# Performance work log

Measured on AMD Instinct MI355X. Metric: run time of the kernel, lower is better.

The kernel has to match this reference:

```python
import jax, jax.numpy as jnp
import numpy as np

NEG_INF = -1e9


def setup_inputs() -> dict:
    key = jax.random.key(0)
    k1, k2, k3, k4 = jax.random.split(key, 4)
    N, F_in, F_out = 8192, 512, 256
    features = jax.random.normal(k1, (N, F_in), dtype=jnp.float32)
    adj = jax.random.randint(k2, (N, N), 0, 2).astype(jnp.float32)
    W = jax.random.normal(k3, (F_in, F_out), dtype=jnp.float32) * 0.05
    a = jax.random.normal(k4, (2 * F_out,), dtype=jnp.float32) * 0.05
    return {"features": features, "adj": adj, "W": W, "a": a}


def reference(features, adj, W, a):
    # h = W @ features  -> [N, F_out]
    h = features @ W
    F_out = h.shape[1]
    a_src, a_dst = a[:F_out], a[F_out:]
    # a^T [h_i ; h_j] decomposes into per-node dot products (same math as
    # the concat+linear in the original, without the [N,N,2F] intermediate).
    e = jax.nn.leaky_relu((h @ a_src)[:, None] + (h @ a_dst)[None, :],
                          negative_slope=0.01)  # [N, N]
    masked_e = e + NEG_INF * (1.0 - adj)
    attention = jax.nn.softmax(masked_e, axis=1)  # row-wise over neighbors j
    output = attention @ h  # [N, F_out]
    return output, attention
```

## Files before the change

### kernel.cpp

```cpp
#include <hip/hip_runtime.h>
#include <hip/hip_bf16.h>

#define N 8192
#define FIN 512
#define FOUT 256

typedef __attribute__((ext_vector_type(8))) short bf16x8;
typedef __attribute__((ext_vector_type(4))) float f32x4;

__device__ __forceinline__ unsigned short f2bf(float x) {
  unsigned int u = __float_as_uint(x);
  return (unsigned short)((u + 0x7FFFu + ((u >> 16) & 1u)) >> 16);
}

__device__ __forceinline__ unsigned int pkbf2(float a, float b) {
  __hip_bfloat162 h = __float22bfloat162_rn(make_float2(a, b));
  unsigned int u;
  __builtin_memcpy(&u, &h, 4);
  return u;
}

__device__ __forceinline__ void load_lds16(const void* g, void* l) {
  __builtin_amdgcn_global_load_lds(
      (const __attribute__((address_space(1))) void*)g,
      (__attribute__((address_space(3))) void*)l, 16, 0, 0);
}

__global__ __launch_bounds__(256) void gat_k1_gemm_h(
    const float* __restrict__ A, const float* __restrict__ W,
    float* __restrict__ h, unsigned short* __restrict__ hT) {
  __shared__ __align__(16) float As[16][68];
  __shared__ __align__(16) float Bs[16][64];
  const int tid = threadIdx.x;
  const int tx = tid & 15, ty = tid >> 4;
  const int nb = blockIdx.x * 64, mb = blockIdx.y * 64;
  float acc[4][4] = {};
  for (int k0 = 0; k0 < FIN; k0 += 16) {
#pragma unroll
    for (int i = 0; i < 4; ++i) {
      int e = tid + 256 * i;
      int m = e >> 4, k = e & 15;
      As[k][m] = A[(size_t)(mb + m) * FIN + k0 + k];
      int n2 = e & 63, k2 = e >> 6;
      Bs[k2][n2] = W[(size_t)(k0 + k2) * FOUT + nb + n2];
    }
    __syncthreads();
#pragma unroll
    for (int k = 0; k < 16; ++k) {
      float4 av = *reinterpret_cast<const float4*>(&As[k][ty * 4]);
      float4 bv = *reinterpret_cast<const float4*>(&Bs[k][tx * 4]);
      float aa[4] = {av.x, av.y, av.z, av.w};
      float bb[4] = {bv.x, bv.y, bv.z, bv.w};
#pragma unroll
      for (int i = 0; i < 4; ++i)
#pragma unroll
        for (int j = 0; j < 4; ++j) acc[i][j] = fmaf(aa[i], bb[j], acc[i][j]);
    }
    __syncthreads();
  }
#pragma unroll
  for (int i = 0; i < 4; ++i) {
    int m = mb + ty * 4 + i;
#pragma unroll
    for (int j = 0; j < 4; ++j) {
      int n = nb + tx * 4 + j;
      h[(size_t)m * FOUT + n] = acc[i][j];
      hT[(size_t)n * N + m] = f2bf(acc[i][j]);
    }
  }
}

__global__ __launch_bounds__(256) void gat_k2_hshd(
    const float* __restrict__ h, const float* __restrict__ a,
    float* __restrict__ hs, float* __restrict__ hd, float* __restrict__ out) {
  const int gid = blockIdx.x * 256 + threadIdx.x;
  *reinterpret_cast<float4*>(out + (size_t)gid * 4) =
      make_float4(0.f, 0.f, 0.f, 0.f);

  const int wid = threadIdx.x >> 6;
  const int lane = threadIdx.x & 63;
  const int row = blockIdx.x * 4 + wid;
  float ps = 0.f, pd = 0.f;
#pragma unroll
  for (int i = 0; i < 4; ++i) {
    int c = lane + 64 * i;
    float v = h[(size_t)row * FOUT + c];
    ps += v * a[c];
    pd += v * a[FOUT + c];
  }
#pragma unroll
  for (int off = 32; off >= 1; off >>= 1) {
    ps += __shfl_down(ps, off);
    pd += __shfl_down(pd, off);
  }
  if (lane == 0) {
    hs[row] = ps;
    hd[row] = pd;
  }
}

__global__ __launch_bounds__(256) void gat_k3_attn(
    const float* __restrict__ adj, const float* __restrict__ hs,
    const float* __restrict__ hd, float* __restrict__ att,
    unsigned short* __restrict__ attB) {
  __shared__ __align__(16) float hd_s[N];
  __shared__ float red[4];
  const int tid = threadIdx.x;
  const int lane = tid & 63, wid = tid >> 6;
#pragma unroll
  for (int i = 0; i < 8; ++i) {
    int j = tid * 4 + 1024 * i;
    *reinterpret_cast<float4*>(&hd_s[j]) =
        *reinterpret_cast<const float4*>(&hd[j]);
  }
  __syncthreads();
  const int row0 = blockIdx.x * 8;
  for (int r = 0; r < 8; ++r) {
    const int row = row0 + r;
    const float hsv = hs[row];
    const float* arow = adj + (size_t)row * N;
    float4 l[8];
    float s = 0.f;
#pragma unroll
    for (int i = 0; i < 8; ++i) {
      int j = tid * 4 + 1024 * i;
      float4 a4 = *reinterpret_cast<const float4*>(&arow[j]);
      float4 h4 = *reinterpret_cast<const float4*>(&hd_s[j]);
      float x0 = hsv + h4.x, x1 = hsv + h4.y;
      float x2 = hsv + h4.z, x3 = hsv + h4.w;
      float4 e;
      e.x = (a4.x != 0.f) ? __expf(fmaxf(x0, 0.01f * x0)) : 0.f;
      e.y = (a4.y != 0.f) ? __expf(fmaxf(x1, 0.01f * x1)) : 0.f;
      e.z = (a4.z != 0.f) ? __expf(fmaxf(x2, 0.01f * x2)) : 0.f;
      e.w = (a4.w != 0.f) ? __expf(fmaxf(x3, 0.01f * x3)) : 0.f;
      l[i] = e;
      s += e.x + e.y + e.z + e.w;
    }
#pragma unroll
    for (int off = 32; off >= 1; off >>= 1) s += __shfl_down(s, off);
    if (lane == 0) red[wid] = s;
    __syncthreads();
    s = red[0] + red[1] + red[2] + red[3];
    __syncthreads();
    const float inv = 1.f / s;
    float* orow = att + (size_t)row * N;
    unsigned short* brow = attB ? attB + (size_t)row * N : nullptr;
#pragma unroll
    for (int i = 0; i < 8; ++i) {
      int j = tid * 4 + 1024 * i;
      float4 e = l[i];
      e.x *= inv; e.y *= inv; e.z *= inv; e.w *= inv;
      *reinterpret_cast<float4*>(&orow[j]) = e;
      if (brow) {
        uint2 pk;
        pk.x = pkbf2(e.x, e.y);
        pk.y = pkbf2(e.z, e.w);
        *reinterpret_cast<uint2*>(&brow[j]) = pk;
      }
    }
  }
}

__global__ __launch_bounds__(512, 4) void gat_k4_out(
    const unsigned short* __restrict__ attB,
    const unsigned short* __restrict__ hT, float* __restrict__ C) {
  __shared__ __align__(16) unsigned short Asb[3 * 64 * 64];
  __shared__ __align__(16) unsigned short Bsb[3 * 128 * 64];
  const int tid = threadIdx.x;
  const int lane = tid & 63;
  const int wid = tid >> 6;
  const int wm = wid & 1, wn = wid >> 1;
  const int g = lane >> 4, rsel = lane & 15;
  const int id = blockIdx.x;
  const int xcd = id & 7, pos = id >> 3;
  const int nh = xcd & 1, kq = (xcd >> 1) & 1, rh = xcd >> 2;
  const int row0 = (rh * 64 + pos) * 64;
  const int nb0 = nh * 128;
  const size_t kbase = (size_t)kq * 4096;

  const int ara = tid >> 3, asl = tid & 7;
  const unsigned short* asrc =
      attB + (size_t)(row0 + ara) * N + kbase + (asl ^ (ara & 7)) * 8;
  const int aofs = tid * 16;
  const unsigned short* bsrc[2];
  int bofs[2];
#pragma unroll
  for (int i = 0; i < 2; ++i) {
    int s = tid + 512 * i;
    int n = s >> 3, sl = s & 7;
    bsrc[i] = hT + (size_t)(nb0 + n) * N + kbase + (sl ^ (n & 7)) * 8;
    bofs[i] = s * 16;
  }

#define STAGE(T, BUF)                                                        \
  do {                                                                       \
    const int kel = (T) * 64;                                                \
    char* Ad = reinterpret_cast<char*>(Asb) + (BUF) * 8192;                  \
    char* Bd = reinterpret_cast<char*>(Bsb) + (BUF) * 16384;                 \
    load_lds16(asrc + kel, Ad + aofs);                                       \
    load_lds16(bsrc[0] + kel, Bd + bofs[0]);                                 \
    load_lds16(bsrc[1] + kel, Bd + bofs[1]);                                 \
  } while (0)

  f32x4 acc[2][2] = {};

  STAGE(0, 0);
  STAGE(1, 1);

  int cur = 0, stg = 2;
  for (int t = 0; t < 64; ++t) {
    if (t < 63)
      asm volatile("s_waitcnt vmcnt(3)" ::: "memory");
    else
      asm volatile("s_waitcnt vmcnt(0)" ::: "memory");
    __builtin_amdgcn_s_barrier();
    __builtin_amdgcn_sched_barrier(0);
    if (t < 62) STAGE(t + 2, stg);
    const char* Ac = reinterpret_cast<const char*>(Asb) + cur * 8192;
    const char* Bc = reinterpret_cast<const char*>(Bsb) + cur * 16384;
#pragma unroll
    for (int ks = 0; ks < 2; ++ks) {
      const int kg = ks * 4 + g;
      bf16x8 af[2], bg[2];
#pragma unroll
      for (int i = 0; i < 2; ++i) {
        int rr = wm * 32 + i * 16 + rsel;
        af[i] = *reinterpret_cast<const bf16x8*>(
            Ac + rr * 128 + ((kg ^ (rr & 7)) << 4));
        int n = wn * 32 + i * 16 + rsel;
        bg[i] = *reinterpret_cast<const bf16x8*>(
            Bc + n * 128 + ((kg ^ (n & 7)) << 4));
      }
#pragma unroll
      for (int i = 0; i < 2; ++i)
#pragma unroll
        for (int f = 0; f < 2; ++f)
          acc[i][f] = __builtin_amdgcn_mfma_f32_16x16x32_bf16(af[i], bg[f],
                                                              acc[i][f], 0, 0, 0);
    }
    cur = (cur == 2) ? 0 : cur + 1;
    stg = (stg == 2) ? 0 : stg + 1;
  }
#undef STAGE
#pragma unroll
  for (int i = 0; i < 2; ++i)
#pragma unroll
    for (int f = 0; f < 2; ++f)
#pragma unroll
      for (int r = 0; r < 4; ++r) {
        int row = row0 + wm * 32 + i * 16 + g * 4 + r;
        int col = nb0 + wn * 32 + f * 16 + rsel;
        atomicAdd(&C[(size_t)row * FOUT + col], acc[i][f][r]);
      }
}

__global__ __launch_bounds__(256, 4) void gat_k4_fb(
    const float* __restrict__ attF, const unsigned short* __restrict__ hT,
    float* __restrict__ C) {
  __shared__ __align__(16) unsigned short As[2][32 * 64];
  __shared__ __align__(16) unsigned short Bs[2][128 * 64];
  const int tid = threadIdx.x;
  const int lane = tid & 63;
  const int wn = tid >> 6;
  const int g = lane >> 4, rsel = lane & 15;
  const int id = blockIdx.x;
  const int xcd = id & 7, j = id >> 3;
  const int nh = xcd >> 2;
  const int row0 = ((xcd & 3) + 4 * j) * 32;
  const int nb0 = nh * 128;

  const float* asrcF[2];
  int awF[2];
#pragma unroll
  for (int i = 0; i < 2; ++i) {
    int e = tid + 256 * i;
    int r = e >> 4, p = e & 15;
    asrcF[i] = attF + (size_t)(row0 + r) * N + p * 4;
    awF[i] = r * 128 + ((((p >> 1) ^ (r & 7)) << 4)) + (p & 1) * 8;
  }
  const unsigned short* bsrc[4];
  int bofs[4];
#pragma unroll
  for (int i = 0; i < 4; ++i) {
    int s = tid + 256 * i;
    int n = s >> 3, sl = s & 7;
    bsrc[i] = hT + (size_t)(nb0 + n) * N + (sl ^ (n & 7)) * 8;
    bofs[i] = s * 16;
  }

  f32x4 acc[2][2] = {};
  float4 aF0, aF1;
  aF0 = *reinterpret_cast<const float4*>(asrcF[0]);
  aF1 = *reinterpret_cast<const float4*>(asrcF[1]);
  {
    uint2 pk;
    pk.x = pkbf2(aF0.x, aF0.y); pk.y = pkbf2(aF0.z, aF0.w);
    *reinterpret_cast<uint2*>(reinterpret_cast<char*>(As[0]) + awF[0]) = pk;
    pk.x = pkbf2(aF1.x, aF1.y); pk.y = pkbf2(aF1.z, aF1.w);
    *reinterpret_cast<uint2*>(reinterpret_cast<char*>(As[0]) + awF[1]) = pk;
  }
#pragma unroll
  for (int i = 0; i < 4; ++i)
    load_lds16(bsrc[i], reinterpret_cast<char*>(Bs[0]) + bofs[i]);
  __syncthreads();

  int cur = 0;
  for (int t = 0; t < 128; ++t) {
    if (t < 127) {
      const int kel = (t + 1) * 64;
      aF0 = *reinterpret_cast<const float4*>(asrcF[0] + kel);
      aF1 = *reinterpret_cast<const float4*>(asrcF[1] + kel);
#pragma unroll
      for (int i = 0; i < 4; ++i)
        load_lds16(bsrc[i] + kel, reinterpret_cast<char*>(Bs[cur ^ 1]) + bofs[i]);
    }
    const char* Ac = reinterpret_cast<const char*>(As[cur]);
    const char* Bc = reinterpret_cast<const char*>(Bs[cur]);
#pragma unroll
    for (int ks = 0; ks < 2; ++ks) {
      bf16x8 af[2], bg[2];
#pragma unroll
      for (int i = 0; i < 2; ++i) {
        int rr = i * 16 + rsel;
        af[i] = *reinterpret_cast<const bf16x8*>(
            Ac + rr * 128 + (((ks * 4 + g) ^ (rr & 7)) << 4));
        int n = wn * 32 + i * 16 + rsel;
        bg[i] = *reinterpret_cast<const bf16x8*>(
            Bc + n * 128 + (((ks * 4 + g) ^ (n & 7)) << 4));
      }
#pragma unroll
      for (int i = 0; i < 2; ++i)
#pragma unroll
        for (int f = 0; f < 2; ++f)
          acc[i][f] = __builtin_amdgcn_mfma_f32_16x16x32_bf16(af[i], bg[f],
                                                              acc[i][f], 0, 0, 0);
    }
    if (t < 127) {
      char* An = reinterpret_cast<char*>(As[cur ^ 1]);
      uint2 pk;
      pk.x = pkbf2(aF0.x, aF0.y); pk.y = pkbf2(aF0.z, aF0.w);
      *reinterpret_cast<uint2*>(An + awF[0]) = pk;
      pk.x = pkbf2(aF1.x, aF1.y); pk.y = pkbf2(aF1.z, aF1.w);
      *reinterpret_cast<uint2*>(An + awF[1]) = pk;
    }
    __syncthreads();
    if (t < 127) cur ^= 1;
  }
#pragma unroll
  for (int i = 0; i < 2; ++i)
#pragma unroll
    for (int f = 0; f < 2; ++f)
#pragma unroll
      for (int r = 0; r < 4; ++r) {
        int row = row0 + i * 16 + g * 4 + r;
        int col = nb0 + wn * 32 + f * 16 + rsel;
        C[(size_t)row * FOUT + col] = acc[i][f][r];
      }
}

extern "C" void kernel_launch(void* const* d_in, const int* in_sizes, int n_in,
                              void* d_out, int out_size, void* d_ws, size_t ws_size,
                              hipStream_t stream) {
  const float* features = (const float*)d_in[0];
  const float* adj = (const float*)d_in[1];
  const float* W = (const float*)d_in[2];
  const float* a = (const float*)d_in[3];

  float* out = (float*)d_out;
  float* att = out + (size_t)N * FOUT;

  char* ws = (char*)d_ws;
  float* h = (float*)ws;
  unsigned short* hT = (unsigned short*)(ws + (size_t)8388608);
  float* hs = (float*)(ws + (size_t)12582912);
  float* hd = hs + N;
  unsigned short* attB = (unsigned short*)(ws + (size_t)16777216);
  const size_t need = 16777216 + (size_t)N * N * 2;
  const bool useB = ws_size >= need;

  hipLaunchKernelGGL(gat_k1_gemm_h, dim3(FOUT / 64, N / 64), dim3(256), 0,
                     stream, features, W, h, hT);
  hipLaunchKernelGGL(gat_k2_hshd, dim3(N / 4), dim3(256), 0, stream, h, a, hs,
                     hd, out);
  hipLaunchKernelGGL(gat_k3_attn, dim3(N / 8), dim3(256), 0, stream, adj, hs,
                     hd, att, useB ? attB : nullptr);
  if (useB)
    hipLaunchKernelGGL(gat_k4_out, dim3(512), dim3(512), 0, stream, attB, hT,
                       out);
  else
    hipLaunchKernelGGL(gat_k4_fb, dim3(512), dim3(256), 0, stream, att, hT,
                       out);
}
```

Before: 264.3 us.

## Replace atomic split-K accumulation with per-split partial buffers and a reduction kernel

The attention·h GEMM now uses 128x128 output tiles with a 4-way K split. Each split writes plain stores into its own partial buffer instead of atomically adding into the zero-initialized output. A new reduction kernel sums the four partials, so the output no longer needs zeroing in the hs/hd kernel. The pipeline also drops from three LDS stages to two with full barriers. The intent is to avoid atomic contention and increase per-block reuse, at the cost of about 32MB of extra partial-buffer traffic and one more launch. The fallback path no longer gets a zeroed output, which may break it if it accumulates.

```diff
diff --git a/kernel.cpp b/kernel.cpp
--- a/kernel.cpp
+++ b/kernel.cpp
@@ -72,11 +72,7 @@
 
 __global__ __launch_bounds__(256) void gat_k2_hshd(
     const float* __restrict__ h, const float* __restrict__ a,
-    float* __restrict__ hs, float* __restrict__ hd, float* __restrict__ out) {
-  const int gid = blockIdx.x * 256 + threadIdx.x;
-  *reinterpret_cast<float4*>(out + (size_t)gid * 4) =
-      make_float4(0.f, 0.f, 0.f, 0.f);
-
+    float* __restrict__ hs, float* __restrict__ hd) {
   const int wid = threadIdx.x >> 6;
   const int lane = threadIdx.x & 63;
   const int row = blockIdx.x * 4 + wid;
@@ -163,25 +159,31 @@
 
 __global__ __launch_bounds__(512, 4) void gat_k4_out(
     const unsigned short* __restrict__ attB,
-    const unsigned short* __restrict__ hT, float* __restrict__ C) {
-  __shared__ __align__(16) unsigned short Asb[3 * 64 * 64];
-  __shared__ __align__(16) unsigned short Bsb[3 * 128 * 64];
+    const unsigned short* __restrict__ hT, float* __restrict__ part) {
+  __shared__ __align__(16) unsigned short As[2][128 * 64];
+  __shared__ __align__(16) unsigned short Bs[2][128 * 64];
   const int tid = threadIdx.x;
   const int lane = tid & 63;
   const int wid = tid >> 6;
-  const int wm = wid & 1, wn = wid >> 1;
+  const int wm = wid >> 2, wn = wid & 3;
   const int g = lane >> 4, rsel = lane & 15;
   const int id = blockIdx.x;
-  const int xcd = id & 7, pos = id >> 3;
-  const int nh = xcd & 1, kq = (xcd >> 1) & 1, rh = xcd >> 2;
-  const int row0 = (rh * 64 + pos) * 64;
+  const int xcd = id & 7;
+  const int nh = xcd & 1, kq = xcd >> 1;
+  const int rb = id >> 3;
+  const int row0 = rb * 128;
   const int nb0 = nh * 128;
-  const size_t kbase = (size_t)kq * 4096;
-
-  const int ara = tid >> 3, asl = tid & 7;
-  const unsigned short* asrc =
-      attB + (size_t)(row0 + ara) * N + kbase + (asl ^ (ara & 7)) * 8;
-  const int aofs = tid * 16;
+  const size_t kbase = (size_t)kq * 2048;
+
+  const unsigned short* asrc[2];
+  int aofs[2];
+#pragma unroll
+  for (int i = 0; i < 2; ++i) {
+    int s = tid + 512 * i;
+    int r = s >> 3, sl = s & 7;
+    asrc[i] = attB + (size_t)(row0 + r) * N + kbase + (sl ^ (r & 7)) * 8;
+    aofs[i] = s * 16;
+  }
   const unsigned short* bsrc[2];
   int bofs[2];
 #pragma unroll
@@ -192,66 +194,81 @@
     bofs[i] = s * 16;
   }
 
-#define STAGE(T, BUF)                                                        \
-  do {                                                                       \
-    const int kel = (T) * 64;                                                \
-    char* Ad = reinterpret_cast<char*>(Asb) + (BUF) * 8192;                  \
-    char* Bd = reinterpret_cast<char*>(Bsb) + (BUF) * 16384;                 \
-    load_lds16(asrc + kel, Ad + aofs);                                       \
-    load_lds16(bsrc[0] + kel, Bd + bofs[0]);                                 \
-    load_lds16(bsrc[1] + kel, Bd + bofs[1]);                                 \
+#define STAGE(T, BUF)                                           \
+  do {                                                          \
+    const int kel = (T) * 64;                                   \
+    char* Ad = reinterpret_cast<char*>(As[(BUF)]);              \
+    char* Bd = reinterpret_cast<char*>(Bs[(BUF)]);              \
+    load_lds16(asrc[0] + kel, Ad + aofs[0]);                    \
+    load_lds16(asrc[1] + kel, Ad + aofs[1]);                    \
+    load_lds16(bsrc[0] + kel, Bd + bofs[0]);                    \
+    load_lds16(bsrc[1] + kel, Bd + bofs[1]);                    \
   } while (0)
 
-  f32x4 acc[2][2] = {};
+  f32x4 acc[4][2] = {};
 
   STAGE(0, 0);
-  STAGE(1, 1);
-
-  int cur = 0, stg = 2;
-  for (int t = 0; t < 64; ++t) {
-    if (t < 63)
-      asm volatile("s_waitcnt vmcnt(3)" ::: "memory");
-    else
-      asm volatile("s_waitcnt vmcnt(0)" ::: "memory");
-    __builtin_amdgcn_s_barrier();
-    __builtin_amdgcn_sched_barrier(0);
-    if (t < 62) STAGE(t + 2, stg);
-    const char* Ac = reinterpret_cast<const char*>(Asb) + cur * 8192;
-    const char* Bc = reinterpret_cast<const char*>(Bsb) + cur * 16384;
+  __syncthreads();
+
+  int cur = 0;
+  for (int t = 0; t < 32; ++t) {
+    if (t < 31) STAGE(t + 1, cur ^ 1);
+    const char* Ac = reinterpret_cast<const char*>(As[cur]);
+    const char* Bc = reinterpret_cast<const char*>(Bs[cur]);
 #pragma unroll
     for (int ks = 0; ks < 2; ++ks) {
       const int kg = ks * 4 + g;
-      bf16x8 af[2], bg[2];
-#pragma unroll
-      for (int i = 0; i < 2; ++i) {
-        int rr = wm * 32 + i * 16 + rsel;
+      bf16x8 af[4], bg[2];
+#pragma unroll
+      for (int i = 0; i < 4; ++i) {
+        int rr = wm * 64 + i * 16 + rsel;
         af[i] = *reinterpret_cast<const bf16x8*>(
             Ac + rr * 128 + ((kg ^ (rr & 7)) << 4));
-        int n = wn * 32 + i * 16 + rsel;
-        bg[i] = *reinterpret_cast<const bf16x8*>(
+      }
+#pragma unroll
+      for (int j = 0; j < 2; ++j) {
+        int n = wn * 32 + j * 16 + rsel;
+        bg[j] = *reinterpret_cast<const bf16x8*>(
             Bc + n * 128 + ((kg ^ (n & 7)) << 4));
       }
 #pragma unroll
-      for (int i = 0; i < 2; ++i)
-#pragma unroll
-        for (int f = 0; f < 2; ++f)
-          acc[i][f] = __builtin_amdgcn_mfma_f32_16x16x32_bf16(af[i], bg[f],
-                                                              acc[i][f], 0, 0, 0);
-    }
-    cur = (cur == 2) ? 0 : cur + 1;
-    stg = (stg == 2) ? 0 : stg + 1;
+      for (int i = 0; i < 4; ++i)
+#pragma unroll
+        for (int j = 0; j < 2; ++j)
+          acc[i][j] = __builtin_amdgcn_mfma_f32_16x16x32_bf16(af[i], bg[j],
+                                                              acc[i][j], 0, 0, 0);
+    }
+    __syncthreads();
+    cur ^= 1;
   }
 #undef STAGE
-#pragma unroll
-  for (int i = 0; i < 2; ++i)
-#pragma unroll
-    for (int f = 0; f < 2; ++f)
+  float* pq = part + (size_t)kq * N * FOUT;
+#pragma unroll
+  for (int i = 0; i < 4; ++i)
+#pragma unroll
+    for (int j = 0; j < 2; ++j)
 #pragma unroll
       for (int r = 0; r < 4; ++r) {
-        int row = row0 + wm * 32 + i * 16 + g * 4 + r;
-        int col = nb0 + wn * 32 + f * 16 + rsel;
-        atomicAdd(&C[(size_t)row * FOUT + col], acc[i][f][r]);
-      }
+        int row = row0 + wm * 64 + i * 16 + g * 4 + r;
+        int col = nb0 + wn * 32 + j * 16 + rsel;
+        pq[(size_t)row * FOUT + col] = acc[i][j][r];
+      }
+}
+
+__global__ __launch_bounds__(256) void gat_k5_red(
+    const float* __restrict__ part, float* __restrict__ out) {
+  const size_t i = ((size_t)blockIdx.x * 256 + threadIdx.x) * 4;
+  const size_t S = (size_t)N * FOUT;
+  float4 s0 = *reinterpret_cast<const float4*>(part + i);
+  float4 s1 = *reinterpret_cast<const float4*>(part + S + i);
+  float4 s2 = *reinterpret_cast<const float4*>(part + 2 * S + i);
+  float4 s3 = *reinterpret_cast<const float4*>(part + 3 * S + i);
+  float4 r;
+  r.x = (s0.x + s1.x) + (s2.x + s3.x);
+  r.y = (s0.y + s1.y) + (s2.y + s3.y);
+  r.z = (s0.z + s1.z) + (s2.z + s3.z);
+  r.w = (s0.w + s1.w) + (s2.w + s3.w);
+  *reinterpret_cast<float4*>(out + i) = r;
 }
 
 __global__ __launch_bounds__(256, 4) void gat_k4_fb(
@@ -375,19 +392,24 @@
   float* hs = (float*)(ws + (size_t)12582912);
   float* hd = hs + N;
   unsigned short* attB = (unsigned short*)(ws + (size_t)16777216);
-  const size_t need = 16777216 + (size_t)N * N * 2;
+  float* part = (float*)(ws + (size_t)16777216 + (size_t)N * N * 2);
+  const size_t need =
+      16777216 + (size_t)N * N * 2 + (size_t)4 * N * FOUT * 4;
   const bool useB = ws_size >= need;
 
   hipLaunchKernelGGL(gat_k1_gemm_h, dim3(FOUT / 64, N / 64), dim3(256), 0,
                      stream, features, W, h, hT);
   hipLaunchKernelGGL(gat_k2_hshd, dim3(N / 4), dim3(256), 0, stream, h, a, hs,
-                     hd, out);
+                     hd);
   hipLaunchKernelGGL(gat_k3_attn, dim3(N / 8), dim3(256), 0, stream, adj, hs,
                      hd, att, useB ? attB : nullptr);
-  if (useB)
+  if (useB) {
     hipLaunchKernelGGL(gat_k4_out, dim3(512), dim3(512), 0, stream, attB, hT,
-                       out);
-  else
+                       part);
+    hipLaunchKernelGGL(gat_k5_red, dim3(N * FOUT / 1024), dim3(256), 0, stream,
+                       part, out);
+  } else {
     hipLaunchKernelGGL(gat_k4_fb, dim3(512), dim3(256), 0, stream, att, hT,
                        out);
-}
+  }
+}
```

Result: faster. 254.9 us (-3.6%).
